# Optimization experiments

Hardware: AMD Instinct MI355X
Metric: run time of the kernel (lower is better)

Reference implementation:

```python
import jax, jax.numpy as jnp
import numpy as np

NEG = -1e9

def setup_inputs() -> dict:
    key = jax.random.key(0)
    ks = jax.random.split(key, 6)
    B, T, H = 32, 2048, 1024
    dec = jax.random.normal(ks[0], (B, H), dtype=jnp.float32)
    enc = jax.random.normal(ks[1], (B, T, H), dtype=jnp.float32)
    mask = jax.random.randint(ks[2], (B, T), 0, 2).astype(jnp.int32)
    scale = 1.0 / np.sqrt(H)
    W_enc = jax.random.normal(ks[3], (H, H), dtype=jnp.float32) * scale
    W_dec = jax.random.normal(ks[4], (H, H), dtype=jnp.float32) * scale
    v = jax.random.normal(ks[5], (H,), dtype=jnp.float32) * scale
    return {"decoder_hidden": dec, "encoder_outputs": enc, "mask": mask,
            "W_enc": W_enc, "W_dec": W_dec, "v": v}

def reference(decoder_hidden, encoder_outputs, mask, W_enc, W_dec, v):
    # enc proj: [B,T,H] @ W_enc^T ; dec proj: [B,H] @ W_dec^T broadcast over T
    enc_p = jnp.einsum('bth,oh->bto', encoder_outputs, W_enc)
    dec_p = jnp.einsum('bh,oh->bo', decoder_hidden, W_dec)[:, None, :]  # [B,1,H]
    energy = jnp.tanh(enc_p + dec_p)                                    # [B,T,H]
    scores = jnp.einsum('bth,h->bt', energy, v)                         # [B,T]
    scores = jnp.where(mask == 0, NEG, scores)
    attn_weights = jax.nn.softmax(scores, axis=1)                       # [B,T]
    context = jnp.einsum('bt,bth->bh', attn_weights, encoder_outputs)   # [B,H]
    return (context, attn_weights)
```

## Files before the change

kernel.cpp:

```cpp
#include <hip/hip_runtime.h>
#include <hip/hip_bf16.h>
#include <stdint.h>

#define B_ 32
#define T_ 2048
#define H_ 1024
#define M_ (B_*T_)

typedef __bf16 bf16x8 __attribute__((ext_vector_type(8)));
typedef float  f32x4  __attribute__((ext_vector_type(4)));
typedef float  f32x16 __attribute__((ext_vector_type(16)));

__device__ __forceinline__ float tanh_fast(float x) {
    float e = __expf(2.0f * x);
    return 1.0f - 2.0f / (e + 1.0f);
}

__global__ __launch_bounds__(256) void k_prep(const float* __restrict__ We,
                                              __bf16* __restrict__ Wt,
                                              const float* __restrict__ dec,
                                              const float* __restrict__ Wd,
                                              float* __restrict__ decp) {
    int bx = blockIdx.x;
    int tid = threadIdx.x;
    if (bx < 512) {
        int tg = bx * 256 + tid;
        int lane = tg & 63;
        int c = (tg >> 6) & 31;
        int s = tg >> 11;
        int o = c * 32 + (lane & 31);
        int k = s * 16 + (lane >> 5) * 8;
        const f32x4* src = (const f32x4*)&We[(size_t)o * H_ + k];
        f32x4 f0 = src[0], f1 = src[1];
        bf16x8 h;
        h[0] = (__bf16)f0[0]; h[1] = (__bf16)f0[1]; h[2] = (__bf16)f0[2]; h[3] = (__bf16)f0[3];
        h[4] = (__bf16)f1[0]; h[5] = (__bf16)f1[1]; h[6] = (__bf16)f1[2]; h[7] = (__bf16)f1[3];
        *(bf16x8*)&Wt[(size_t)tg * 8] = h;
    } else {
        int bxd = bx - 512;
        int b = bxd & 31, oc = bxd >> 5;
        int o = oc * 64 + (tid >> 2);
        int kq = tid & 3;
        const f32x4* wr = (const f32x4*)&Wd[(size_t)o * H_ + kq * 256];
        const f32x4* dr = (const f32x4*)&dec[(size_t)b * H_ + kq * 256];
        f32x4 s4 = {0.f, 0.f, 0.f, 0.f};
#pragma unroll 8
        for (int i = 0; i < 64; ++i) s4 += wr[i] * dr[i];
        float s = s4[0] + s4[1] + s4[2] + s4[3];
        s += __shfl_xor(s, 1);
        s += __shfl_xor(s, 2);
        if (kq == 0) decp[b * H_ + o] = s;
    }
}

__global__ __launch_bounds__(256, 4) void k_scores(const float* __restrict__ enc,
                                                   const float* __restrict__ decp,
                                                   const __bf16* __restrict__ Wt,
                                                   const float* __restrict__ v,
                                                   float* __restrict__ scores) {
    __shared__ __bf16 A_lds[64 * 32 * 8];
    __shared__ float red[4][64];

    const int tid = threadIdx.x;
    const int w = tid >> 6, lane = tid & 63;
    const int l5 = lane & 31, q2 = lane >> 5;

    const int bx = blockIdx.x;
    const int xs = bx & 7;
    const int q = bx >> 3;
    const int nt = q & 3;
    const int rg = (q >> 2) * 8 + xs;
    const int m0 = rg * 64;
    const int b = m0 >> 11;
    const int cg0 = nt * 8 + w * 2;

    float dp[2], vvv[2];
#pragma unroll
    for (int ct = 0; ct < 2; ++ct) {
        int col = (cg0 + ct) * 32 + l5;
        dp[ct]  = decp[b * H_ + col];
        vvv[ct] = v[col];
    }

    f32x16 acc[2][2];
#pragma unroll
    for (int rt = 0; rt < 2; ++rt)
#pragma unroll
        for (int ct = 0; ct < 2; ++ct)
#pragma unroll
            for (int g = 0; g < 16; ++g)
                acc[rt][ct][g] = dp[ct];

    const int ko_s = tid & 31;
    const int rbase = (tid >> 5) * 8;

    bf16x8 b_cur[2];
#pragma unroll
    for (int ct = 0; ct < 2; ++ct)
        b_cur[ct] = *(const bf16x8*)&Wt[(((size_t)0 * 32 + cg0 + ct) * 64 + lane) * 8];

#pragma unroll 1
    for (int kc = 0; kc < 4; ++kc) {
        {
            const float* sp0 = &enc[(size_t)(m0 + rbase) * H_ + kc * 256 + ko_s * 8];
#pragma unroll
            for (int i = 0; i < 8; ++i) {
                const f32x4* s4 = (const f32x4*)(sp0 + (size_t)i * H_);
                f32x4 f0 = s4[0], f1 = s4[1];
                bf16x8 h;
                h[0] = (__bf16)f0[0]; h[1] = (__bf16)f0[1]; h[2] = (__bf16)f0[2]; h[3] = (__bf16)f0[3];
                h[4] = (__bf16)f1[0]; h[5] = (__bf16)f1[1]; h[6] = (__bf16)f1[2]; h[7] = (__bf16)f1[3];
                int row = rbase + i;
                int cell = row * 32 + ((ko_s & 24) | ((ko_s ^ row) & 7));
                *(bf16x8*)&A_lds[cell * 8] = h;
            }
        }
        __syncthreads();

#pragma unroll
        for (int sl = 0; sl < 16; ++sl) {
            int s = kc * 16 + sl;
            int sn = (s + 1) & 63;
            bf16x8 b_nxt[2];
#pragma unroll
            for (int ct = 0; ct < 2; ++ct)
                b_nxt[ct] = *(const bf16x8*)&Wt[(((size_t)sn * 32 + cg0 + ct) * 64 + lane) * 8];

            bf16x8 af[2];
#pragma unroll
            for (int rt = 0; rt < 2; ++rt) {
                int row = rt * 32 + l5;
                int ko = sl * 2 + q2;
                int cell = row * 32 + ((ko & 24) | ((ko ^ row) & 7));
                af[rt] = *(const bf16x8*)&A_lds[cell * 8];
            }

            acc[0][0] = __builtin_amdgcn_mfma_f32_32x32x16_bf16(af[0], b_cur[0], acc[0][0], 0, 0, 0);
            acc[0][1] = __builtin_amdgcn_mfma_f32_32x32x16_bf16(af[0], b_cur[1], acc[0][1], 0, 0, 0);
            acc[1][0] = __builtin_amdgcn_mfma_f32_32x32x16_bf16(af[1], b_cur[0], acc[1][0], 0, 0, 0);
            acc[1][1] = __builtin_amdgcn_mfma_f32_32x32x16_bf16(af[1], b_cur[1], acc[1][1], 0, 0, 0);

            b_cur[0] = b_nxt[0];
            b_cur[1] = b_nxt[1];
        }
        __syncthreads();
    }

    float sp[2][16];
#pragma unroll
    for (int rt = 0; rt < 2; ++rt)
#pragma unroll
        for (int g = 0; g < 16; ++g)
            sp[rt][g] = tanh_fast(acc[rt][0][g]) * vvv[0] + tanh_fast(acc[rt][1][g]) * vvv[1];

#pragma unroll
    for (int rt = 0; rt < 2; ++rt)
#pragma unroll
        for (int g = 0; g < 16; ++g) {
            float s = sp[rt][g];
            s += __shfl_xor(s, 1);
            s += __shfl_xor(s, 2);
            s += __shfl_xor(s, 4);
            s += __shfl_xor(s, 8);
            s += __shfl_xor(s, 16);
            sp[rt][g] = s;
        }

    if (l5 == 0) {
#pragma unroll
        for (int rt = 0; rt < 2; ++rt)
#pragma unroll
            for (int g = 0; g < 16; ++g) {
                int row = rt * 32 + (g & 3) + 8 * (g >> 2) + 4 * q2;
                red[w][row] = sp[rt][g];
            }
    }
    __syncthreads();
    if (tid < 64) {
        float s = red[0][tid] + red[1][tid] + red[2][tid] + red[3][tid];
        atomicAdd(&scores[m0 + tid], s);
    }
}

__global__ __launch_bounds__(256) void k_softmax(const float* __restrict__ scores,
                                                 const int* __restrict__ mask,
                                                 float* __restrict__ attn) {
    int b = blockIdx.x;
    int tid = threadIdx.x;
    int w = tid >> 6, lane = tid & 63;
    __shared__ float sm[2][4];
    float val[8];
    float mx = -3e38f;
#pragma unroll
    for (int ii = 0; ii < 8; ++ii) {
        int t = tid + ii * 256;
        float s = scores[b * T_ + t];
        s = (mask[b * T_ + t] == 0) ? -1e9f : s;
        val[ii] = s;
        mx = fmaxf(mx, s);
    }
#pragma unroll
    for (int m = 1; m <= 32; m <<= 1) mx = fmaxf(mx, __shfl_xor(mx, m));
    if (lane == 0) sm[0][w] = mx;
    __syncthreads();
    mx = fmaxf(fmaxf(sm[0][0], sm[0][1]), fmaxf(sm[0][2], sm[0][3]));
    float lsum = 0.f;
#pragma unroll
    for (int ii = 0; ii < 8; ++ii) {
        val[ii] = __expf(val[ii] - mx);
        lsum += val[ii];
    }
#pragma unroll
    for (int m = 1; m <= 32; m <<= 1) lsum += __shfl_xor(lsum, m);
    if (lane == 0) sm[1][w] = lsum;
    __syncthreads();
    float inv = 1.0f / (sm[1][0] + sm[1][1] + sm[1][2] + sm[1][3]);
#pragma unroll
    for (int ii = 0; ii < 8; ++ii)
        attn[b * T_ + tid + ii * 256] = val[ii] * inv;
}

__global__ __launch_bounds__(512) void k_context(const float* __restrict__ enc,
                                                 const float* __restrict__ attn,
                                                 float* __restrict__ ctx) {
    __shared__ f32x4 cred[8][32];
    int bx = blockIdx.x;
    int b = bx >> 3, hc = bx & 7;
    int tid = threadIdx.x;
    int wv = tid >> 6, lane = tid & 63;
    int l5 = lane & 31, tq2 = lane >> 5;
    int h = hc * 128 + l5 * 4;
    const float* ap = &attn[b * T_ + wv * 256 + tq2];
    const float* ep = &enc[((size_t)b * T_ + wv * 256 + tq2) * H_ + h];
    f32x4 acc = {0.f, 0.f, 0.f, 0.f};
#pragma unroll 8
    for (int i = 0; i < 128; ++i) {
        float a = ap[2 * i];
        f32x4 e = *(const f32x4*)(ep + (size_t)2 * i * H_);
        acc += a * e;
    }
#pragma unroll
    for (int c = 0; c < 4; ++c) acc[c] += __shfl_xor(acc[c], 32);
    if (tq2 == 0) cred[wv][l5] = acc;
    __syncthreads();
    if (tid < 32) {
        f32x4 r = cred[0][tid];
#pragma unroll
        for (int j = 1; j < 8; ++j) r += cred[j][tid];
        *(f32x4*)&ctx[b * H_ + hc * 128 + tid * 4] = r;
    }
}

extern "C" void kernel_launch(void* const* d_in, const int* in_sizes, int n_in,
                              void* d_out, int out_size, void* d_ws, size_t ws_size,
                              hipStream_t stream) {
    (void)in_sizes; (void)n_in; (void)out_size; (void)ws_size;
    const float* dec  = (const float*)d_in[0];
    const float* enc  = (const float*)d_in[1];
    const int*   mask = (const int*)d_in[2];
    const float* We   = (const float*)d_in[3];
    const float* Wd   = (const float*)d_in[4];
    const float* v    = (const float*)d_in[5];

    float* out = (float*)d_out;
    char* ws = (char*)d_ws;
    float*  decp   = (float*)ws;
    float*  scores = (float*)(ws + 131072);
    __bf16* Wt     = (__bf16*)(ws + 131072 + 262144);

    hipMemsetAsync(scores, 0, (size_t)M_ * sizeof(float), stream);

    k_prep   <<<1024, 256, 0, stream>>>(We, Wt, dec, Wd, decp);
    k_scores <<<4096, 256, 0, stream>>>(enc, decp, Wt, v, scores);
    k_softmax<<<32, 256, 0, stream>>>(scores, mask, out + B_ * H_);
    k_context<<<256, 512, 0, stream>>>(enc, out + B_ * H_, out);
}
```

Measured before the change: 588.5 us.

## Double-buffer encoder tile in LDS and replace atomics with partial score buffers

The scores kernel now double-buffers its bf16 A tile in LDS. It prefetches the next K-chunk of encoder rows into registers while MFMAs run on the current chunk, and uses a deeper 4-stage register prefetch for weight fragments plus 2-ahead LDS fragment reads. The per-column-tile atomicAdd into scores is replaced by writes to four separate partial buffers, which softmax sums, so the memset launch goes away. Occupancy hint drops from 4 to 2 blocks per CU to fit the extra registers and LDS, which may reduce latency hiding.

```diff
diff --git a/kernel.cpp b/kernel.cpp
--- a/kernel.cpp
+++ b/kernel.cpp
@@ -14,6 +14,13 @@
 __device__ __forceinline__ float tanh_fast(float x) {
     float e = __expf(2.0f * x);
     return 1.0f - 2.0f / (e + 1.0f);
+}
+
+__device__ __forceinline__ bf16x8 cvt2(f32x4 f0, f32x4 f1) {
+    bf16x8 h;
+    h[0] = (__bf16)f0[0]; h[1] = (__bf16)f0[1]; h[2] = (__bf16)f0[2]; h[3] = (__bf16)f0[3];
+    h[4] = (__bf16)f1[0]; h[5] = (__bf16)f1[1]; h[6] = (__bf16)f1[2]; h[7] = (__bf16)f1[3];
+    return h;
 }
 
 __global__ __launch_bounds__(256) void k_prep(const float* __restrict__ We,
@@ -31,11 +38,7 @@
         int o = c * 32 + (lane & 31);
         int k = s * 16 + (lane >> 5) * 8;
         const f32x4* src = (const f32x4*)&We[(size_t)o * H_ + k];
-        f32x4 f0 = src[0], f1 = src[1];
-        bf16x8 h;
-        h[0] = (__bf16)f0[0]; h[1] = (__bf16)f0[1]; h[2] = (__bf16)f0[2]; h[3] = (__bf16)f0[3];
-        h[4] = (__bf16)f1[0]; h[5] = (__bf16)f1[1]; h[6] = (__bf16)f1[2]; h[7] = (__bf16)f1[3];
-        *(bf16x8*)&Wt[(size_t)tg * 8] = h;
+        *(bf16x8*)&Wt[(size_t)tg * 8] = cvt2(src[0], src[1]);
     } else {
         int bxd = bx - 512;
         int b = bxd & 31, oc = bxd >> 5;
@@ -53,12 +56,12 @@
     }
 }
 
-__global__ __launch_bounds__(256, 4) void k_scores(const float* __restrict__ enc,
+__global__ __launch_bounds__(256, 2) void k_scores(const float* __restrict__ enc,
                                                    const float* __restrict__ decp,
                                                    const __bf16* __restrict__ Wt,
                                                    const float* __restrict__ v,
-                                                   float* __restrict__ scores) {
-    __shared__ __bf16 A_lds[64 * 32 * 8];
+                                                   float* __restrict__ scores_p) {
+    __shared__ __bf16 A_lds[2][64 * 32 * 8];
     __shared__ float red[4][64];
 
     const int tid = threadIdx.x;
@@ -93,55 +96,89 @@
 
     const int ko_s = tid & 31;
     const int rbase = (tid >> 5) * 8;
-
-    bf16x8 b_cur[2];
-#pragma unroll
-    for (int ct = 0; ct < 2; ++ct)
-        b_cur[ct] = *(const bf16x8*)&Wt[(((size_t)0 * 32 + cg0 + ct) * 64 + lane) * 8];
+    const float* sbase = &enc[(size_t)(m0 + rbase) * H_ + ko_s * 8];
+
+    {
+#pragma unroll
+        for (int i = 0; i < 8; ++i) {
+            const f32x4* s4 = (const f32x4*)(sbase + (size_t)i * H_);
+            int row = rbase + i;
+            int cell = row * 32 + ((ko_s & 24) | ((ko_s ^ row) & 7));
+            *(bf16x8*)&A_lds[0][cell * 8] = cvt2(s4[0], s4[1]);
+        }
+    }
+    __syncthreads();
+
+    bf16x8 bb[4][2];
+#pragma unroll
+    for (int p = 0; p < 4; ++p)
+#pragma unroll
+        for (int ct = 0; ct < 2; ++ct)
+            bb[p][ct] = *(const bf16x8*)&Wt[(((size_t)p * 32 + cg0 + ct) * 64 + lane) * 8];
 
 #pragma unroll 1
     for (int kc = 0; kc < 4; ++kc) {
-        {
-            const float* sp0 = &enc[(size_t)(m0 + rbase) * H_ + kc * 256 + ko_s * 8];
+        const __bf16* buf = A_lds[kc & 1];
+
+        f32x4 sr[8][2];
+        if (kc < 3) {
+            const float* sp0 = sbase + (size_t)(kc + 1) * 256;
 #pragma unroll
             for (int i = 0; i < 8; ++i) {
                 const f32x4* s4 = (const f32x4*)(sp0 + (size_t)i * H_);
-                f32x4 f0 = s4[0], f1 = s4[1];
-                bf16x8 h;
-                h[0] = (__bf16)f0[0]; h[1] = (__bf16)f0[1]; h[2] = (__bf16)f0[2]; h[3] = (__bf16)f0[3];
-                h[4] = (__bf16)f1[0]; h[5] = (__bf16)f1[1]; h[6] = (__bf16)f1[2]; h[7] = (__bf16)f1[3];
+                sr[i][0] = s4[0];
+                sr[i][1] = s4[1];
+            }
+        }
+
+        bf16x8 af[2][2];
+#pragma unroll
+        for (int p = 0; p < 2; ++p)
+#pragma unroll
+            for (int rt = 0; rt < 2; ++rt) {
+                int row = rt * 32 + l5;
+                int ko = p * 2 + q2;
+                int cell = row * 32 + ((ko & 24) | ((ko ^ row) & 7));
+                af[p][rt] = *(const bf16x8*)&buf[cell * 8];
+            }
+
+#pragma unroll
+        for (int sl = 0; sl < 16; ++sl) {
+            const int s = kc * 16 + sl;
+            bf16x8 a0 = af[sl & 1][0], a1 = af[sl & 1][1];
+            bf16x8 w0 = bb[s & 3][0],  w1 = bb[s & 3][1];
+
+            {
+                int sn = (s + 4) & 63;
+#pragma unroll
+                for (int ct = 0; ct < 2; ++ct)
+                    bb[s & 3][ct] = *(const bf16x8*)&Wt[(((size_t)sn * 32 + cg0 + ct) * 64 + lane) * 8];
+            }
+            {
+                int sl2 = (sl + 2) & 15;
+#pragma unroll
+                for (int rt = 0; rt < 2; ++rt) {
+                    int row = rt * 32 + l5;
+                    int ko = sl2 * 2 + q2;
+                    int cell = row * 32 + ((ko & 24) | ((ko ^ row) & 7));
+                    af[sl & 1][rt] = *(const bf16x8*)&buf[cell * 8];
+                }
+            }
+
+            acc[0][0] = __builtin_amdgcn_mfma_f32_32x32x16_bf16(a0, w0, acc[0][0], 0, 0, 0);
+            acc[0][1] = __builtin_amdgcn_mfma_f32_32x32x16_bf16(a0, w1, acc[0][1], 0, 0, 0);
+            acc[1][0] = __builtin_amdgcn_mfma_f32_32x32x16_bf16(a1, w0, acc[1][0], 0, 0, 0);
+            acc[1][1] = __builtin_amdgcn_mfma_f32_32x32x16_bf16(a1, w1, acc[1][1], 0, 0, 0);
+        }
+
+        if (kc < 3) {
+            __bf16* dst = A_lds[(kc + 1) & 1];
+#pragma unroll
+            for (int i = 0; i < 8; ++i) {
                 int row = rbase + i;
                 int cell = row * 32 + ((ko_s & 24) | ((ko_s ^ row) & 7));
-                *(bf16x8*)&A_lds[cell * 8] = h;
-            }
-        }
-        __syncthreads();
-
-#pragma unroll
-        for (int sl = 0; sl < 16; ++sl) {
-            int s = kc * 16 + sl;
-            int sn = (s + 1) & 63;
-            bf16x8 b_nxt[2];
-#pragma unroll
-            for (int ct = 0; ct < 2; ++ct)
-                b_nxt[ct] = *(const bf16x8*)&Wt[(((size_t)sn * 32 + cg0 + ct) * 64 + lane) * 8];
-
-            bf16x8 af[2];
-#pragma unroll
-            for (int rt = 0; rt < 2; ++rt) {
-                int row = rt * 32 + l5;
-                int ko = sl * 2 + q2;
-                int cell = row * 32 + ((ko & 24) | ((ko ^ row) & 7));
-                af[rt] = *(const bf16x8*)&A_lds[cell * 8];
-            }
-
-            acc[0][0] = __builtin_amdgcn_mfma_f32_32x32x16_bf16(af[0], b_cur[0], acc[0][0], 0, 0, 0);
-            acc[0][1] = __builtin_amdgcn_mfma_f32_32x32x16_bf16(af[0], b_cur[1], acc[0][1], 0, 0, 0);
-            acc[1][0] = __builtin_amdgcn_mfma_f32_32x32x16_bf16(af[1], b_cur[0], acc[1][0], 0, 0, 0);
-            acc[1][1] = __builtin_amdgcn_mfma_f32_32x32x16_bf16(af[1], b_cur[1], acc[1][1], 0, 0, 0);
-
-            b_cur[0] = b_nxt[0];
-            b_cur[1] = b_nxt[1];
+                *(bf16x8*)&dst[cell * 8] = cvt2(sr[i][0], sr[i][1]);
+            }
         }
         __syncthreads();
     }
@@ -178,11 +215,11 @@
     __syncthreads();
     if (tid < 64) {
         float s = red[0][tid] + red[1][tid] + red[2][tid] + red[3][tid];
-        atomicAdd(&scores[m0 + tid], s);
-    }
-}
-
-__global__ __launch_bounds__(256) void k_softmax(const float* __restrict__ scores,
+        scores_p[nt * M_ + m0 + tid] = s;
+    }
+}
+
+__global__ __launch_bounds__(256) void k_softmax(const float* __restrict__ scores_p,
                                                  const int* __restrict__ mask,
                                                  float* __restrict__ attn) {
     int b = blockIdx.x;
@@ -193,9 +230,9 @@
     float mx = -3e38f;
 #pragma unroll
     for (int ii = 0; ii < 8; ++ii) {
-        int t = tid + ii * 256;
-        float s = scores[b * T_ + t];
-        s = (mask[b * T_ + t] == 0) ? -1e9f : s;
+        int idx = b * T_ + tid + ii * 256;
+        float s = scores_p[idx] + scores_p[M_ + idx] + scores_p[2 * M_ + idx] + scores_p[3 * M_ + idx];
+        s = (mask[idx] == 0) ? -1e9f : s;
         val[ii] = s;
         mx = fmaxf(mx, s);
     }
@@ -264,14 +301,12 @@
 
     float* out = (float*)d_out;
     char* ws = (char*)d_ws;
-    float*  decp   = (float*)ws;
-    float*  scores = (float*)(ws + 131072);
-    __bf16* Wt     = (__bf16*)(ws + 131072 + 262144);
-
-    hipMemsetAsync(scores, 0, (size_t)M_ * sizeof(float), stream);
+    float*  decp     = (float*)ws;
+    float*  scores_p = (float*)(ws + 131072);
+    __bf16* Wt       = (__bf16*)(ws + 131072 + 1048576);
 
     k_prep   <<<1024, 256, 0, stream>>>(We, Wt, dec, Wd, decp);
-    k_scores <<<4096, 256, 0, stream>>>(enc, decp, Wt, v, scores);
-    k_softmax<<<32, 256, 0, stream>>>(scores, mask, out + B_ * H_);
+    k_scores <<<4096, 256, 0, stream>>>(enc, decp, Wt, v, scores_p);
+    k_softmax<<<32, 256, 0, stream>>>(scores_p, mask, out + B_ * H_);
     k_context<<<256, 512, 0, stream>>>(enc, out + B_ * H_, out);
 }
```

Result: no change. 582.1 us (-1.1%).
